# Kernel optimization log

Measured on AMD Instinct MI355X. Metric: run time of the kernel, lower is better.

Reference implementation:

```python
import jax, jax.numpy as jnp
import numpy as np

N = 50000      # nodes
E = 800000     # edges
D_IN = 128
HID = 128
L = 3          # local_layers
EPS = 1e-5     # LayerNorm eps


def setup_inputs() -> dict:
    key = jax.random.key(0)
    ks = jax.random.split(key, 8)
    s_in = 1.0 / np.sqrt(D_IN)
    s_h = 1.0 / np.sqrt(HID)
    return {
        "x": jax.random.normal(ks[0], (N, D_IN), jnp.float32),
        "edge_index": jax.random.randint(ks[1], (2, E), 0, N, dtype=jnp.int64),
        "lin_in_w": jax.random.normal(ks[2], (D_IN, HID), jnp.float32) * s_in,
        "lin_in_b": jnp.zeros((HID,), jnp.float32),
        "conv_w": jax.random.normal(ks[3], (L, HID, HID), jnp.float32) * s_h,
        "conv_b": jnp.zeros((L, HID), jnp.float32),
        "lin_w": jax.random.normal(ks[4], (L, HID, HID), jnp.float32) * s_h,
        "lin_b": jnp.zeros((L, HID), jnp.float32),
        "ln_g": jnp.ones((L, HID), jnp.float32),
        "ln_b": jnp.zeros((L, HID), jnp.float32),
    }


def reference(x, edge_index, lin_in_w, lin_in_b, conv_w, conv_b, lin_w, lin_b, ln_g, ln_b):
    # GCNConv(normalize=True, add_self_loops=True): augment with self loops
    loops = jnp.arange(N, dtype=edge_index.dtype)
    src = jnp.concatenate([edge_index[0], loops])
    dst = jnp.concatenate([edge_index[1], loops])
    deg = jax.ops.segment_sum(jnp.ones_like(dst, x.dtype), dst, num_segments=N)
    dinv = jnp.where(deg > 0, jax.lax.rsqrt(deg), 0.0)
    norm = dinv[src] * dinv[dst]  # [E+N]

    # pre_linear (dropout p=0, eval)
    x = x @ lin_in_w + lin_in_b

    x_final = jnp.zeros((N, HID), x.dtype)
    for i in range(L):
        h = x @ conv_w[i]
        agg = jax.ops.segment_sum(h[src] * norm[:, None], dst, num_segments=N) + conv_b[i]
        # residual linear
        x = agg + x @ lin_w[i] + lin_b[i]
        # LayerNorm
        mu = jnp.mean(x, axis=-1, keepdims=True)
        var = jnp.var(x, axis=-1, keepdims=True)
        x = (x - mu) * jax.lax.rsqrt(var + EPS) * ln_g[i] + ln_b[i]
        x = jax.nn.relu(x)
        x_final = x_final + x  # JK sum
    return x_final
```

## Files before the change

### kernel.cpp

```cpp
#include <hip/hip_runtime.h>

#define HID 128
#define LN_EPS 1e-5f

typedef __attribute__((ext_vector_type(8))) short bf16x8;
typedef __attribute__((ext_vector_type(4))) float f32x4;

__device__ __forceinline__ ushort f2bf(float v) {
  union { float f; uint u; } x; x.f = v;
  uint r = x.u + 0x7fffu + ((x.u >> 16) & 1u);
  return (ushort)(r >> 16);
}
__device__ __forceinline__ float bf2f(ushort u) {
  union { uint u; float f; } x; x.u = (uint)u << 16; return x.f;
}


__global__ void k_init(int* __restrict__ cnt, int n) {
  int i = blockIdx.x * 256 + threadIdx.x;
  if (i < n) cnt[i] = 0;
}

__global__ void k_count(const int* __restrict__ dst, int* __restrict__ cnt,
                        int* __restrict__ rank, int E) {
  int e = blockIdx.x * 256 + threadIdx.x;
  if (e < E) rank[e] = atomicAdd(&cnt[dst[e]], 1);
}

__global__ void k_dinv(const int* __restrict__ cnt, float* __restrict__ dinv, int n) {
  int i = blockIdx.x * 256 + threadIdx.x;
  if (i < n) dinv[i] = rsqrtf((float)cnt[i] + 1.0f);
}

__global__ void k_bsum(const int* __restrict__ cnt, int* __restrict__ bsum, int n) {
  __shared__ int red[256];
  int b = blockIdx.x, t = threadIdx.x;
  int i = b * 512 + t * 2;
  int s = ((i < n) ? cnt[i] : 0) + ((i + 1 < n) ? cnt[i + 1] : 0);
  red[t] = s;
  __syncthreads();
  for (int off = 128; off > 0; off >>= 1) {
    if (t < off) red[t] += red[t + off];
    __syncthreads();
  }
  if (t == 0) bsum[b] = red[0];
}

__global__ void k_bscan(int* __restrict__ bsum, int nb) {
  __shared__ int buf[1024];
  int t = threadIdx.x;
  int v = (t < nb) ? bsum[t] : 0;
  buf[t] = v;
  __syncthreads();
  for (int off = 1; off < 1024; off <<= 1) {
    int u = (t >= off) ? buf[t - off] : 0;
    __syncthreads();
    buf[t] += u;
    __syncthreads();
  }
  if (t < nb) bsum[t] = buf[t] - v;
}

__global__ void k_rowstart(const int* __restrict__ cnt, const int* __restrict__ bsum,
                           int* __restrict__ row_start, int n) {
  __shared__ int buf[256];
  int b = blockIdx.x, t = threadIdx.x;
  int i = b * 512 + t * 2;
  int c0 = (i < n) ? cnt[i] : 0;
  int c1 = (i + 1 < n) ? cnt[i + 1] : 0;
  int s = c0 + c1;
  buf[t] = s;
  __syncthreads();
  int mine = s;
  for (int off = 1; off < 256; off <<= 1) {
    int u = (t >= off) ? buf[t - off] : 0;
    __syncthreads();
    buf[t] += u;
    __syncthreads();
  }
  int ex = buf[t] - mine + bsum[b];
  if (i < n) row_start[i] = ex;
  if (i + 1 < n) row_start[i + 1] = ex + c0;
}

__global__ void k_scatter(const int* __restrict__ src, const int* __restrict__ dst,
                          const int* __restrict__ row_start, const int* __restrict__ rank,
                          const float* __restrict__ dinv,
                          uint2* __restrict__ rec, int E) {
  int e = blockIdx.x * 256 + threadIdx.x;
  if (e < E) {
    int d = dst[e], s = src[e];
    int pos = row_start[d] + rank[e];
    union { float f; uint u; } w; w.f = dinv[s] * dinv[d];
    rec[pos] = make_uint2((uint)s, w.u);
  }
}

__global__ void k_prep_w(const float* __restrict__ lin_in_w,
                         const float* __restrict__ conv_w, const float* __restrict__ lin_w,
                         const float* __restrict__ conv_b, const float* __restrict__ lin_b,
                         ushort* __restrict__ wt_in, ushort* __restrict__ wt_l,
                         float* __restrict__ bsum, int L) {
  int tid = blockIdx.x * 256 + threadIdx.x;
  int total = L * 128 * 256;
  if (tid < total) {
    int l = tid >> 15;
    int idx = tid & 32767;
    int n = idx >> 12;
    int r = idx & 4095;
    int ks = r >> 9;
    int r2 = r & 511;
    int lane = r2 >> 3;
    int j = r2 & 7;
    int k2 = ks * 32 + (lane >> 4) * 8 + j;
    int c = n * 16 + (lane & 15);
    float v = (k2 < 128) ? conv_w[((size_t)l * 128 + k2) * 128 + c]
                         : lin_w[((size_t)l * 128 + (k2 - 128)) * 128 + c];
    wt_l[tid] = f2bf(v);
  }
  if (tid < 128 * 128) {
    int n = tid >> 11;
    int r = tid & 2047;
    int ks = r >> 9;
    int r2 = r & 511;
    int lane = r2 >> 3;
    int j = r2 & 7;
    int k = ks * 32 + (lane >> 4) * 8 + j;
    int c = n * 16 + (lane & 15);
    wt_in[tid] = f2bf(lin_in_w[k * 128 + c]);
  }
  if (tid < L * 128) bsum[tid] = conv_b[tid] + lin_b[tid];
}

__global__ void k_agg(const ushort* __restrict__ X, const int* __restrict__ row_start,
                      const int* __restrict__ cnt, const float* __restrict__ dinv,
                      const uint2* __restrict__ rec, ushort* __restrict__ Sout, int n) {
  int node = blockIdx.x * 4 + (threadIdx.x >> 6);
  if (node >= n) return;
  int lane = threadIdx.x & 63;
  float dv = dinv[node];
  uint v = *reinterpret_cast<const uint*>(X + (size_t)node * HID + lane * 2);
  float ax = dv * dv * bf2f((ushort)(v & 0xffff));
  float ay = dv * dv * bf2f((ushort)(v >> 16));
  int start = row_start[node];
  int m = cnt[node];
  int last = start + m - 1;
  for (int e = 0; e < m; e += 4) {
    int i0 = start + e;
    uint2 r0 = rec[i0];
    uint2 r1 = rec[min(i0 + 1, last)];
    uint2 r2 = rec[min(i0 + 2, last)];
    uint2 r3 = rec[min(i0 + 3, last)];
    uint u0 = *reinterpret_cast<const uint*>(X + (size_t)r0.x * HID + lane * 2);
    uint u1 = *reinterpret_cast<const uint*>(X + (size_t)r1.x * HID + lane * 2);
    uint u2 = *reinterpret_cast<const uint*>(X + (size_t)r2.x * HID + lane * 2);
    uint u3 = *reinterpret_cast<const uint*>(X + (size_t)r3.x * HID + lane * 2);
    union { uint u; float f; } w0, w1, w2, w3;
    w0.u = r0.y;
    w1.u = (e + 1 < m) ? r1.y : 0u;
    w2.u = (e + 2 < m) ? r2.y : 0u;
    w3.u = (e + 3 < m) ? r3.y : 0u;
    ax = fmaf(w0.f, bf2f((ushort)(u0 & 0xffff)), ax);
    ay = fmaf(w0.f, bf2f((ushort)(u0 >> 16)), ay);
    ax = fmaf(w1.f, bf2f((ushort)(u1 & 0xffff)), ax);
    ay = fmaf(w1.f, bf2f((ushort)(u1 >> 16)), ay);
    ax = fmaf(w2.f, bf2f((ushort)(u2 & 0xffff)), ax);
    ay = fmaf(w2.f, bf2f((ushort)(u2 >> 16)), ay);
    ax = fmaf(w3.f, bf2f((ushort)(u3 & 0xffff)), ax);
    ay = fmaf(w3.f, bf2f((ushort)(u3 >> 16)), ay);
  }
  uint o = (uint)f2bf(ax) | ((uint)f2bf(ay) << 16);
  *reinterpret_cast<uint*>(Sout + (size_t)node * HID + lane * 2) = o;
}


__global__ void __launch_bounds__(256, 2)
k_gemm_in(const float* __restrict__ Xin, const ushort* __restrict__ WtF,
          const float* __restrict__ bias, ushort* __restrict__ Xout, int nrows) {
  __shared__ float lds[4 * 16 * 132];
  const int tid = threadIdx.x;
  const int wid = tid >> 6, lane = tid & 63;
  const int lr = lane & 15, lg = lane >> 4;
  const int r0 = blockIdx.x * 64 + wid * 16;
  const int arow = r0 + lr;
  const bool rowok = arow < nrows;

  bf16x8 a[4];
  {
    const float* xp = Xin + (size_t)arow * HID + lg * 8;
#pragma unroll
    for (int ks = 0; ks < 4; ks++) {
      bf16x8 t;
#pragma unroll
      for (int i = 0; i < 8; i++) t[i] = 0;
      if (rowok) {
        float4 u0 = *reinterpret_cast<const float4*>(xp + ks * 32);
        float4 u1 = *reinterpret_cast<const float4*>(xp + ks * 32 + 4);
        t[0] = (short)f2bf(u0.x); t[1] = (short)f2bf(u0.y);
        t[2] = (short)f2bf(u0.z); t[3] = (short)f2bf(u0.w);
        t[4] = (short)f2bf(u1.x); t[5] = (short)f2bf(u1.y);
        t[6] = (short)f2bf(u1.z); t[7] = (short)f2bf(u1.w);
      }
      a[ks] = t;
    }
  }

  f32x4 acc[8];
#pragma unroll
  for (int n = 0; n < 8; n++) acc[n] = f32x4{0.f, 0.f, 0.f, 0.f};

  const ushort* wb = WtF + lane * 8;
#pragma unroll
  for (int n = 0; n < 8; n++)
#pragma unroll
    for (int ks = 0; ks < 4; ks++) {
      bf16x8 b = *reinterpret_cast<const bf16x8*>(wb + (n * 4 + ks) * 512);
      acc[n] = __builtin_amdgcn_mfma_f32_16x16x32_bf16(a[ks], b, acc[n], 0, 0, 0);
    }

  float* T = lds + wid * (16 * 132);
#pragma unroll
  for (int n = 0; n < 8; n++)
#pragma unroll
    for (int q = 0; q < 4; q++)
      T[(lg * 4 + q) * 132 + n * 16 + lr] = acc[n][q];

  const int c0 = lg * 32;
  const float* Trow = T + lr * 132 + c0;
  const int orow = r0 + lr;
  if (orow < nrows) {
    ushort* xo = Xout + (size_t)orow * HID + c0;
    uint pk[16];
#pragma unroll
    for (int j = 0; j < 8; j++) {
      float4 t = *reinterpret_cast<const float4*>(Trow + j * 4);
      float4 b4 = *reinterpret_cast<const float4*>(bias + c0 + j * 4);
      float o0 = t.x + b4.x, o1 = t.y + b4.y, o2 = t.z + b4.z, o3 = t.w + b4.w;
      pk[j * 2 + 0] = (uint)f2bf(o0) | ((uint)f2bf(o1) << 16);
      pk[j * 2 + 1] = (uint)f2bf(o2) | ((uint)f2bf(o3) << 16);
    }
#pragma unroll
    for (int j = 0; j < 4; j++)
      *reinterpret_cast<uint4*>(xo + j * 8) =
          make_uint4(pk[j * 4 + 0], pk[j * 4 + 1], pk[j * 4 + 2], pk[j * 4 + 3]);
  }
}

__global__ void __launch_bounds__(256, 2)
k_layer(const ushort* __restrict__ S, const ushort* __restrict__ Xin,
        ushort* __restrict__ Xout,
        const ushort* __restrict__ WtF, const float* __restrict__ bsum,
        const float* __restrict__ gamma, const float* __restrict__ beta, int nrows) {
  __shared__ float lds[4 * 16 * 132];
  const int tid = threadIdx.x;
  const int wid = tid >> 6, lane = tid & 63;
  const int lr = lane & 15, lg = lane >> 4;
  const int r0 = blockIdx.x * 64 + wid * 16;
  const int arow = r0 + lr;
  const bool rowok = arow < nrows;

  bf16x8 a[8];
  {
    const ushort* sp = S + (size_t)arow * HID + lg * 8;
    const ushort* xp = Xin + (size_t)arow * HID + lg * 8;
    bf16x8 z;
#pragma unroll
    for (int i = 0; i < 8; i++) z[i] = 0;
#pragma unroll
    for (int ks = 0; ks < 4; ks++)
      a[ks] = rowok ? *reinterpret_cast<const bf16x8*>(sp + ks * 32) : z;
#pragma unroll
    for (int ks = 0; ks < 4; ks++)
      a[4 + ks] = rowok ? *reinterpret_cast<const bf16x8*>(xp + ks * 32) : z;
  }

  f32x4 acc[8];
#pragma unroll
  for (int n = 0; n < 8; n++) acc[n] = f32x4{0.f, 0.f, 0.f, 0.f};

  const ushort* wb = WtF + lane * 8;
#pragma unroll
  for (int n = 0; n < 8; n++)
#pragma unroll
    for (int ks = 0; ks < 8; ks++) {
      bf16x8 b = *reinterpret_cast<const bf16x8*>(wb + (n * 8 + ks) * 512);
      acc[n] = __builtin_amdgcn_mfma_f32_16x16x32_bf16(a[ks], b, acc[n], 0, 0, 0);
    }

  float* T = lds + wid * (16 * 132);
#pragma unroll
  for (int n = 0; n < 8; n++)
#pragma unroll
    for (int q = 0; q < 4; q++)
      T[(lg * 4 + q) * 132 + n * 16 + lr] = acc[n][q];

  const int c0 = lg * 32;
  const float* Trow = T + lr * 132 + c0;
  float v[32];
  float sum = 0.f, sq = 0.f;
#pragma unroll
  for (int j = 0; j < 8; j++) {
    float4 t = *reinterpret_cast<const float4*>(Trow + j * 4);
    float4 b4 = *reinterpret_cast<const float4*>(bsum + c0 + j * 4);
    float x0 = t.x + b4.x, x1 = t.y + b4.y, x2 = t.z + b4.z, x3 = t.w + b4.w;
    v[j * 4 + 0] = x0; v[j * 4 + 1] = x1; v[j * 4 + 2] = x2; v[j * 4 + 3] = x3;
    sum += (x0 + x1) + (x2 + x3);
    sq = fmaf(x0, x0, sq); sq = fmaf(x1, x1, sq);
    sq = fmaf(x2, x2, sq); sq = fmaf(x3, x3, sq);
  }
  sum += __shfl_xor(sum, 16); sq += __shfl_xor(sq, 16);
  sum += __shfl_xor(sum, 32); sq += __shfl_xor(sq, 32);
  const float mean = sum * (1.f / 128.f);
  const float rstd = rsqrtf(sq * (1.f / 128.f) - mean * mean + LN_EPS);

  const int orow = r0 + lr;
  if (orow < nrows) {
    ushort* xo = Xout + (size_t)orow * HID + c0;
    uint pk[16];
#pragma unroll
    for (int j = 0; j < 8; j++) {
      float4 g4 = *reinterpret_cast<const float4*>(gamma + c0 + j * 4);
      float4 b4 = *reinterpret_cast<const float4*>(beta + c0 + j * 4);
      float o0 = fmaxf(fmaf((v[j * 4 + 0] - mean) * rstd, g4.x, b4.x), 0.f);
      float o1 = fmaxf(fmaf((v[j * 4 + 1] - mean) * rstd, g4.y, b4.y), 0.f);
      float o2 = fmaxf(fmaf((v[j * 4 + 2] - mean) * rstd, g4.z, b4.z), 0.f);
      float o3 = fmaxf(fmaf((v[j * 4 + 3] - mean) * rstd, g4.w, b4.w), 0.f);
      pk[j * 2 + 0] = (uint)f2bf(o0) | ((uint)f2bf(o1) << 16);
      pk[j * 2 + 1] = (uint)f2bf(o2) | ((uint)f2bf(o3) << 16);
    }
#pragma unroll
    for (int j = 0; j < 4; j++)
      *reinterpret_cast<uint4*>(xo + j * 8) =
          make_uint4(pk[j * 4 + 0], pk[j * 4 + 1], pk[j * 4 + 2], pk[j * 4 + 3]);
  }
}

__global__ void k_jk(const ushort* __restrict__ a, const ushort* __restrict__ b,
                     const ushort* __restrict__ c, float* __restrict__ out, int total8) {
  int i = blockIdx.x * 256 + threadIdx.x;
  if (i >= total8) return;
  uint4 ua = *reinterpret_cast<const uint4*>(a + (size_t)i * 8);
  uint4 ub = *reinterpret_cast<const uint4*>(b + (size_t)i * 8);
  uint4 uc = *reinterpret_cast<const uint4*>(c + (size_t)i * 8);
  float o[8];
  const uint pa[4] = {ua.x, ua.y, ua.z, ua.w};
  const uint pb[4] = {ub.x, ub.y, ub.z, ub.w};
  const uint pc[4] = {uc.x, uc.y, uc.z, uc.w};
#pragma unroll
  for (int j = 0; j < 4; j++) {
    o[j * 2 + 0] = bf2f((ushort)(pa[j] & 0xffff)) + bf2f((ushort)(pb[j] & 0xffff)) +
                   bf2f((ushort)(pc[j] & 0xffff));
    o[j * 2 + 1] = bf2f((ushort)(pa[j] >> 16)) + bf2f((ushort)(pb[j] >> 16)) +
                   bf2f((ushort)(pc[j] >> 16));
  }
  float* op = out + (size_t)i * 8;
  *reinterpret_cast<float4*>(op) = make_float4(o[0], o[1], o[2], o[3]);
  *reinterpret_cast<float4*>(op + 4) = make_float4(o[4], o[5], o[6], o[7]);
}


extern "C" void kernel_launch(void* const* d_in, const int* in_sizes, int n_in,
                              void* d_out, int out_size, void* d_ws, size_t ws_size,
                              hipStream_t stream) {
  const float* x_in     = (const float*)d_in[0];
  const int*   edge     = (const int*)d_in[1];
  const float* lin_in_w = (const float*)d_in[2];
  const float* lin_in_b = (const float*)d_in[3];
  const float* conv_w   = (const float*)d_in[4];
  const float* conv_b   = (const float*)d_in[5];
  const float* lin_w    = (const float*)d_in[6];
  const float* lin_b    = (const float*)d_in[7];
  const float* ln_g     = (const float*)d_in[8];
  const float* ln_b     = (const float*)d_in[9];

  int N = in_sizes[0] / HID;
  int E = in_sizes[1] / 2;
  int L = in_sizes[4] / (HID * HID);

  const int* src = edge;
  const int* dst = edge + E;

  char* ws = (char*)d_ws;
  size_t off = 0;
  auto alloc = [&](size_t bytes) -> void* {
    void* p = (void*)(ws + off);
    off += (bytes + 255) & ~(size_t)255;
    return p;
  };
  int*    cnt       = (int*)alloc((size_t)N * 4);
  int*    rank      = (int*)alloc((size_t)E * 4);
  int*    row_start = (int*)alloc((size_t)N * 4);
  float*  dinv      = (float*)alloc((size_t)N * 4);
  int*    blocksum  = (int*)alloc(4096);
  uint2*  rec       = (uint2*)alloc((size_t)E * 8);
  ushort* xb0       = (ushort*)alloc((size_t)N * HID * 2);
  ushort* xb1       = (ushort*)alloc((size_t)N * HID * 2);
  ushort* xb2       = (ushort*)alloc((size_t)N * HID * 2);
  ushort* sbuf      = (ushort*)alloc((size_t)N * HID * 2);
  ushort* wt_in     = (ushort*)alloc((size_t)128 * 128 * 2);
  ushort* wt_l      = (ushort*)alloc((size_t)L * 128 * 256 * 2);
  float*  bsum      = (float*)alloc((size_t)L * 128 * 4);
  (void)ws_size; (void)n_in; (void)out_size;

  int nb_n = (N + 255) / 256;
  int nb_e = (E + 255) / 256;
  int nbs  = (N + 511) / 512;
  int nb_g = (N + 63) / 64;
  int nb_w = (L * 128 * 256 + 255) / 256;
  int total8 = N * HID / 8;
  int nb_j = (total8 + 255) / 256;

  k_init<<<nb_n, 256, 0, stream>>>(cnt, N);
  k_count<<<nb_e, 256, 0, stream>>>(dst, cnt, rank, E);
  k_dinv<<<nb_n, 256, 0, stream>>>(cnt, dinv, N);
  k_bsum<<<nbs, 256, 0, stream>>>(cnt, blocksum, N);
  k_bscan<<<1, 1024, 0, stream>>>(blocksum, nbs);
  k_rowstart<<<nbs, 256, 0, stream>>>(cnt, blocksum, row_start, N);
  k_scatter<<<nb_e, 256, 0, stream>>>(src, dst, row_start, rank, dinv, rec, E);
  k_prep_w<<<nb_w, 256, 0, stream>>>(lin_in_w, conv_w, lin_w, conv_b, lin_b,
                                     wt_in, wt_l, bsum, L);

  k_gemm_in<<<nb_g, 256, 0, stream>>>(x_in, wt_in, lin_in_b, xb0, N);

  ushort* xin_b[3]  = {xb0, xb1, xb2};
  ushort* xout_b[3] = {xb1, xb2, xb0};
  for (int i = 0; i < L; i++) {
    k_agg<<<(N + 3) / 4, 256, 0, stream>>>(xin_b[i], row_start, cnt, dinv, rec, sbuf, N);
    k_layer<<<nb_g, 256, 0, stream>>>(sbuf, xin_b[i], xout_b[i],
        wt_l + (size_t)i * 128 * 256, bsum + (size_t)i * 128,
        ln_g + (size_t)i * HID, ln_b + (size_t)i * HID, N);
  }
  k_jk<<<nb_j, 256, 0, stream>>>(xb1, xb2, xb0, (float*)d_out, total8);
}
```

Before: 360.3 us.

## Split aggregation over column chunks and edge-parallel lanes with shuffle reduction

The gather-aggregate kernel now assigns each wavefront one node and one 32-column chunk (four blocks per node group). Eight lane groups each handle different edges and load 8 bytes per lane, and partial sums are combined with xor shuffles before lane group zero adds the self-loop term and stores. This raises memory-level parallelism for low-degree nodes and uses wider loads, at the cost of four times more edge-record reads, shuffle reductions, and idle lanes on the final store. Edge records are read and outputs written with nontemporal hints.

Result: slower. 522.3 us (+44.9%).

```diff
diff --git a/kernel.cpp b/kernel.cpp
--- a/kernel.cpp
+++ b/kernel.cpp
@@ -135,42 +135,60 @@
 __global__ void k_agg(const ushort* __restrict__ X, const int* __restrict__ row_start,
                       const int* __restrict__ cnt, const float* __restrict__ dinv,
                       const uint2* __restrict__ rec, ushort* __restrict__ Sout, int n) {
-  int node = blockIdx.x * 4 + (threadIdx.x >> 6);
+  const int chunk = blockIdx.x & 3;
+  const int node = (blockIdx.x >> 2) * 4 + (threadIdx.x >> 6);
   if (node >= n) return;
-  int lane = threadIdx.x & 63;
-  float dv = dinv[node];
-  uint v = *reinterpret_cast<const uint*>(X + (size_t)node * HID + lane * 2);
-  float ax = dv * dv * bf2f((ushort)(v & 0xffff));
-  float ay = dv * dv * bf2f((ushort)(v >> 16));
-  int start = row_start[node];
-  int m = cnt[node];
-  int last = start + m - 1;
-  for (int e = 0; e < m; e += 4) {
-    int i0 = start + e;
-    uint2 r0 = rec[i0];
-    uint2 r1 = rec[min(i0 + 1, last)];
-    uint2 r2 = rec[min(i0 + 2, last)];
-    uint2 r3 = rec[min(i0 + 3, last)];
-    uint u0 = *reinterpret_cast<const uint*>(X + (size_t)r0.x * HID + lane * 2);
-    uint u1 = *reinterpret_cast<const uint*>(X + (size_t)r1.x * HID + lane * 2);
-    uint u2 = *reinterpret_cast<const uint*>(X + (size_t)r2.x * HID + lane * 2);
-    uint u3 = *reinterpret_cast<const uint*>(X + (size_t)r3.x * HID + lane * 2);
-    union { uint u; float f; } w0, w1, w2, w3;
-    w0.u = r0.y;
-    w1.u = (e + 1 < m) ? r1.y : 0u;
-    w2.u = (e + 2 < m) ? r2.y : 0u;
-    w3.u = (e + 3 < m) ? r3.y : 0u;
-    ax = fmaf(w0.f, bf2f((ushort)(u0 & 0xffff)), ax);
-    ay = fmaf(w0.f, bf2f((ushort)(u0 >> 16)), ay);
-    ax = fmaf(w1.f, bf2f((ushort)(u1 & 0xffff)), ax);
-    ay = fmaf(w1.f, bf2f((ushort)(u1 >> 16)), ay);
-    ax = fmaf(w2.f, bf2f((ushort)(u2 & 0xffff)), ax);
-    ay = fmaf(w2.f, bf2f((ushort)(u2 >> 16)), ay);
-    ax = fmaf(w3.f, bf2f((ushort)(u3 & 0xffff)), ax);
-    ay = fmaf(w3.f, bf2f((ushort)(u3 >> 16)), ay);
-  }
-  uint o = (uint)f2bf(ax) | ((uint)f2bf(ay) << 16);
-  *reinterpret_cast<uint*>(Sout + (size_t)node * HID + lane * 2) = o;
+  const int lane = threadIdx.x & 63;
+  const int esub = lane >> 3;
+  const int cg   = lane & 7;
+  const int colb = chunk * 32 + cg * 4;
+
+  float a0 = 0.f, a1 = 0.f, a2 = 0.f, a3 = 0.f;
+  const int start = row_start[node];
+  const int m = cnt[node];
+  const int last = start + m - 1;
+  const ulong* recq = reinterpret_cast<const ulong*>(rec);
+
+  for (int e = 0; e < m; e += 16) {
+    int ia = start + e + esub;
+    int ib = ia + 8;
+    ulong qa = __builtin_nontemporal_load(recq + min(ia, last));
+    ulong qb = __builtin_nontemporal_load(recq + min(ib, last));
+    uint sa = (uint)qa, sb = (uint)qb;
+    union { uint u; float f; } wa, wb;
+    wa.u = (e + esub < m) ? (uint)(qa >> 32) : 0u;
+    wb.u = (e + 8 + esub < m) ? (uint)(qb >> 32) : 0u;
+    uint2 ua = *reinterpret_cast<const uint2*>(X + (size_t)sa * HID + colb);
+    uint2 ub = *reinterpret_cast<const uint2*>(X + (size_t)sb * HID + colb);
+    a0 = fmaf(wa.f, bf2f((ushort)(ua.x & 0xffff)), a0);
+    a1 = fmaf(wa.f, bf2f((ushort)(ua.x >> 16)), a1);
+    a2 = fmaf(wa.f, bf2f((ushort)(ua.y & 0xffff)), a2);
+    a3 = fmaf(wa.f, bf2f((ushort)(ua.y >> 16)), a3);
+    a0 = fmaf(wb.f, bf2f((ushort)(ub.x & 0xffff)), a0);
+    a1 = fmaf(wb.f, bf2f((ushort)(ub.x >> 16)), a1);
+    a2 = fmaf(wb.f, bf2f((ushort)(ub.y & 0xffff)), a2);
+    a3 = fmaf(wb.f, bf2f((ushort)(ub.y >> 16)), a3);
+  }
+#pragma unroll
+  for (int s = 8; s < 64; s <<= 1) {
+    a0 += __shfl_xor(a0, s);
+    a1 += __shfl_xor(a1, s);
+    a2 += __shfl_xor(a2, s);
+    a3 += __shfl_xor(a3, s);
+  }
+  if (esub == 0) {
+    float dv = dinv[node];
+    float d2 = dv * dv;
+    uint2 u = *reinterpret_cast<const uint2*>(X + (size_t)node * HID + colb);
+    a0 = fmaf(d2, bf2f((ushort)(u.x & 0xffff)), a0);
+    a1 = fmaf(d2, bf2f((ushort)(u.x >> 16)), a1);
+    a2 = fmaf(d2, bf2f((ushort)(u.y & 0xffff)), a2);
+    a3 = fmaf(d2, bf2f((ushort)(u.y >> 16)), a3);
+    ulong o = (ulong)((uint)f2bf(a0) | ((uint)f2bf(a1) << 16)) |
+              ((ulong)((uint)f2bf(a2) | ((uint)f2bf(a3) << 16)) << 32);
+    __builtin_nontemporal_store(o,
+        reinterpret_cast<ulong*>(Sout + (size_t)node * HID + colb));
+  }
 }
 
 
@@ -407,6 +425,7 @@
   int nbs  = (N + 511) / 512;
   int nb_g = (N + 63) / 64;
   int nb_w = (L * 128 * 256 + 255) / 256;
+  int nb_a = 4 * ((N + 3) / 4);
   int total8 = N * HID / 8;
   int nb_j = (total8 + 255) / 256;
 
@@ -425,7 +444,7 @@
   ushort* xin_b[3]  = {xb0, xb1, xb2};
   ushort* xout_b[3] = {xb1, xb2, xb0};
   for (int i = 0; i < L; i++) {
-    k_agg<<<(N + 3) / 4, 256, 0, stream>>>(xin_b[i], row_start, cnt, dinv, rec, sbuf, N);
+    k_agg<<<nb_a, 256, 0, stream>>>(xin_b[i], row_start, cnt, dinv, rec, sbuf, N);
     k_layer<<<nb_g, 256, 0, stream>>>(sbuf, xin_b[i], xout_b[i],
         wt_l + (size_t)i * 128 * 256, bsum + (size_t)i * 128,
         ln_g + (size_t)i * HID, ln_b + (size_t)i * HID, N);
```
